# Optimization experiments

Hardware: AMD Instinct MI355X
Metric: run time of the kernel (lower is better)

Reference implementation:

```python
import jax, jax.numpy as jnp
import numpy as np

D_MODEL = 1024
N_HEADS = 16
HEAD_DIM = D_MODEL // N_HEADS


def setup_inputs() -> dict:
    key = jax.random.key(0)
    ks = jax.random.split(key, 9)
    B, T, S, D = 4, 2048, 512, D_MODEL
    sc = 1.0 / np.sqrt(D)
    return {
        "x": jax.random.normal(ks[0], (B, T, D), dtype=jnp.float32),
        "context": jax.random.normal(ks[1], (B, S, D), dtype=jnp.float32),
        "context_mask": jnp.ones((B, S), dtype=bool),
        "Wq": jax.random.normal(ks[2], (D, D), dtype=jnp.float32) * sc,
        "bq": jnp.zeros((D,), dtype=jnp.float32),
        "Wkv": jax.random.normal(ks[3], (D, 2 * D), dtype=jnp.float32) * sc,
        "bkv": jnp.zeros((2 * D,), dtype=jnp.float32),
        "Wp": jax.random.normal(ks[4], (D, D), dtype=jnp.float32) * sc,
        "bp": jnp.zeros((D,), dtype=jnp.float32),
    }


def reference(x, context, context_mask, Wq, bq, Wkv, bkv, Wp, bp):
    B, T, D = x.shape
    S = context.shape[1]
    H, Hd = N_HEADS, HEAD_DIM
    # projections
    q = (x @ Wq + bq).reshape(B, T, H, Hd).transpose(0, 2, 1, 3)          # [B,H,T,Hd]
    kv = (context @ Wkv + bkv).reshape(B, S, 2, H, Hd)
    k = kv[:, :, 0].transpose(0, 2, 1, 3)                                  # [B,H,S,Hd]
    v = kv[:, :, 1].transpose(0, 2, 1, 3)                                  # [B,H,S,Hd]
    # scaled dot-product attention with context mask
    scores = jnp.einsum("bhtd,bhsd->bhts", q, k) / np.sqrt(Hd)            # [B,H,T,S]
    neg_inf = jnp.finfo(scores.dtype).min
    scores = jnp.where(context_mask[:, None, None, :], scores, neg_inf)
    attn = jax.nn.softmax(scores, axis=-1)
    # dropout is identity in eval mode (p applied only in training)
    out = jnp.einsum("bhts,bhsd->bthd", attn, v).reshape(B, T, D)
    return out @ Wp + bp
```

## Files before the change

kernel.cpp:

```cpp
#include <hip/hip_runtime.h>

typedef __bf16 bf16x8 __attribute__((ext_vector_type(8)));
typedef float  f32x4  __attribute__((ext_vector_type(4)));
typedef float  f32x16 __attribute__((ext_vector_type(16)));
typedef unsigned int u32x2 __attribute__((ext_vector_type(2)));

#define MFMA(a, b, c)   __builtin_amdgcn_mfma_f32_16x16x32_bf16((a), (b), (c), 0, 0, 0)
#define MFMA32(a, b, c) __builtin_amdgcn_mfma_f32_32x32x16_bf16((a), (b), (c), 0, 0, 0)

#define GLL(g, l) __builtin_amdgcn_global_load_lds(                                  \
    (const __attribute__((address_space(1))) void*)(g),                              \
    (__attribute__((address_space(3))) void*)(l), 16, 0, 0)

#define BB 4
#define TT 2048
#define SS 512
#define DM 1024
#define NH 16
#define HD 64

__device__ __forceinline__ unsigned short f2bh(float f) {
    __bf16 h = (__bf16)f;
    union { __bf16 h; unsigned short u; } v; v.h = h;
    return v.u;
}

__device__ __forceinline__ unsigned int pk2(float a, float b) {
    return (unsigned int)f2bh(a) | ((unsigned int)f2bh(b) << 16);
}

__device__ __forceinline__ void pl32swap(unsigned int& a, unsigned int& b) {
    u32x2 r = __builtin_amdgcn_permlane32_swap(a, b, false, false);
    a = r[0]; b = r[1];
}

__device__ __forceinline__ float fexp2(float x) {
    float e;
    asm("v_exp_f32 %0, %1" : "=v"(e) : "v"(x));
    return e;
}

__device__ __forceinline__ void tcast_tile(const float* __restrict__ in,
                                           unsigned short* __restrict__ out,
                                           int K, int N, int n0, int k0,
                                           float (*tile)[33], int tid) {
    int tx = tid & 31, ty = tid >> 5;
#pragma unroll
    for (int r = 0; r < 32; r += 8)
        tile[ty + r][tx] = in[(k0 + ty + r) * N + n0 + tx];
    __syncthreads();
    int r2 = tid >> 3, cg = (tid & 7) * 4;
    ushort4 o;
    o.x = f2bh(tile[cg + 0][r2]);
    o.y = f2bh(tile[cg + 1][r2]);
    o.z = f2bh(tile[cg + 2][r2]);
    o.w = f2bh(tile[cg + 3][r2]);
    *(ushort4*)&out[(n0 + r2) * K + k0 + cg] = o;
}

__global__ __launch_bounds__(256)
void prep(const float4* __restrict__ x, const float4* __restrict__ ctx,
          const unsigned int* __restrict__ mw,
          const float* __restrict__ Wq, const float* __restrict__ Wkv,
          const float* __restrict__ Wp,
          ushort4* __restrict__ Xbf, ushort4* __restrict__ Cbf,
          unsigned short* __restrict__ WqT, unsigned short* __restrict__ WkvT,
          unsigned short* __restrict__ WpT, float* __restrict__ mbias) {
    __shared__ float tile[32][33];
    __shared__ int flags[2];
    const int bid = blockIdx.x, tid = threadIdx.x;
    if (bid < 8192) {
        int i = bid * 256 + tid;
        float4 v = x[i];
        ushort4 o; o.x = f2bh(v.x); o.y = f2bh(v.y); o.z = f2bh(v.z); o.w = f2bh(v.w);
        Xbf[i] = o;
    } else if (bid < 10240) {
        int i = (bid - 8192) * 256 + tid;
        float4 v = ctx[i];
        ushort4 o; o.x = f2bh(v.x); o.y = f2bh(v.y); o.z = f2bh(v.z); o.w = f2bh(v.w);
        Cbf[i] = o;
    } else if (bid < 11264) {
        int loc = bid - 10240;
        tcast_tile(Wq, WqT, DM, DM, (loc & 31) * 32, (loc >> 5) * 32, tile, tid);
    } else if (bid < 13312) {
        int loc = bid - 11264;
        tcast_tile(Wkv, WkvT, DM, 2 * DM, (loc & 63) * 32, (loc >> 6) * 32, tile, tid);
    } else if (bid < 14336) {
        int loc = bid - 13312;
        tcast_tile(Wp, WpT, DM, DM, (loc & 31) * 32, (loc >> 5) * 32, tile, tid);
    } else {
        if (tid == 0) { flags[0] = 1; flags[1] = 1; }
        __syncthreads();
        int okI = 1, okF = 1;
        for (int i = tid; i < 512; i += 256) {
            unsigned int w = mw[i];
            if (w > 1u) okI = 0;
            if (w != 0u && w != 0x3f800000u) okF = 0;
        }
        if (!okI) atomicAnd(&flags[0], 0);
        if (!okF) atomicAnd(&flags[1], 0);
        __syncthreads();
        bool wordLayout = (flags[0] != 0) || (flags[1] != 0);
        const unsigned char* mb = (const unsigned char*)mw;
        for (int s = tid; s < BB * SS; s += 256) {
            bool on = wordLayout ? (mw[s] != 0u) : (mb[s] != 0);
            mbias[s] = on ? 0.0f : -1e38f;
        }
    }
}

__device__ __forceinline__ void gemm_core(
    const unsigned short* __restrict__ A, const unsigned short* __restrict__ Bt,
    int K, int m0, int n0, unsigned short* As, unsigned short* Bs,
    f32x4 (*acc)[4]) {
    const int tid = threadIdx.x;
    const int l = tid & 63;
    const int quad = l >> 4, col = l & 15;
    const int w = tid >> 6;
    const int wm = (w & 1) * 64, wn = (w >> 1) * 64;
    const int arow = tid >> 3;
    const int apiece = (tid & 7) ^ (arow & 7);
    const unsigned short* Ab = A + (size_t)(m0 + arow) * K + apiece * 8;
    const unsigned short* Bb = Bt + (size_t)(n0 + arow) * K + apiece * 8;

    for (int k0 = 0; k0 < K; k0 += 64) {
        __syncthreads();
#pragma unroll
        for (int g = 0; g < 4; ++g)
            GLL(Ab + k0 + g * 32 * K, &As[g * 2048 + tid * 8]);
#pragma unroll
        for (int g = 0; g < 4; ++g)
            GLL(Bb + k0 + g * 32 * K, &Bs[g * 2048 + tid * 8]);
        __syncthreads();
#pragma unroll
        for (int k32 = 0; k32 < 2; ++k32) {
            bf16x8 af[4], bfr[4];
#pragma unroll
            for (int i = 0; i < 4; i++) {
                int rr = wm + i * 16 + col;
                af[i] = *(const bf16x8*)&As[rr * 64 + (((k32 * 4 + quad) ^ (rr & 7)) * 8)];
            }
#pragma unroll
            for (int j = 0; j < 4; j++) {
                int rr = wn + j * 16 + col;
                bfr[j] = *(const bf16x8*)&Bs[rr * 64 + (((k32 * 4 + quad) ^ (rr & 7)) * 8)];
            }
#pragma unroll
            for (int i = 0; i < 4; i++)
#pragma unroll
                for (int j = 0; j < 4; j++) acc[i][j] = MFMA(af[i], bfr[j], acc[i][j]);
        }
    }
}

__global__ __launch_bounds__(256, 3)
void gemm_qkv(const unsigned short* __restrict__ Xbf, const unsigned short* __restrict__ WqT,
              const float* __restrict__ bq, unsigned short* __restrict__ Qb,
              const unsigned short* __restrict__ Cbf, const unsigned short* __restrict__ WkvT,
              const float* __restrict__ bkv, unsigned short* __restrict__ Kb,
              unsigned short* __restrict__ Vtb) {
    __shared__ __align__(16) unsigned short S[16640];
    unsigned short* As = S;
    unsigned short* Bs = S + 8192;
    const int tid = threadIdx.x;
    const int l = tid & 63;
    const int quad = l >> 4, col = l & 15;
    const int w = tid >> 6;
    const int wm = (w & 1) * 64, wn = (w >> 1) * 64;
    const int bid = blockIdx.x;

    const f32x4 zero = {0.f, 0.f, 0.f, 0.f};
    f32x4 acc[4][4];
#pragma unroll
    for (int i = 0; i < 4; i++)
#pragma unroll
        for (int j = 0; j < 4; j++) acc[i][j] = zero;

    if (bid < 512) {
        const int xg = bid & 7, t = bid >> 3;
        const int m0 = (xg + 8 * (t & 7)) * 128;
        const int n0 = (t >> 3) * 128;
        gemm_core(Xbf, WqT, DM, m0, n0, As, Bs, acc);
        const float QS = 0.125f * 1.4426950408889634f;
#pragma unroll
        for (int i = 0; i < 4; i++) {
#pragma unroll
            for (int j = 0; j < 4; j++) {
                int n = n0 + wn + j * 16 + col;
                int mb = m0 + wm + i * 16 + quad * 4;
                float bv = bq[n];
#pragma unroll
                for (int ii = 0; ii < 4; ii++)
                    Qb[(mb + ii) * DM + n] = f2bh((acc[i][j][ii] + bv) * QS);
            }
        }
    } else {
        const int loc = bid - 512;
        const int xg = loc & 7, t = loc >> 3;
        const int m0 = (xg + 8 * (t & 1)) * 128;
        const int n0 = (t >> 1) * 128;
        gemm_core(Cbf, WkvT, DM, m0, n0, As, Bs, acc);
        if (n0 < 1024) {
#pragma unroll
            for (int i = 0; i < 4; i++) {
#pragma unroll
                for (int j = 0; j < 4; j++) {
                    int n = n0 + wn + j * 16 + col;
                    int mb = m0 + wm + i * 16 + quad * 4;
                    float bv = bkv[n];
                    int h = n >> 6, d = n & 63;
#pragma unroll
                    for (int ii = 0; ii < 4; ii++) {
                        int m = mb + ii; int b = m >> 9, s = m & 511;
                        Kb[(((b * NH + h) * SS) + s) * HD + d] = f2bh(acc[ii == ii ? i : i][j][ii] + bv);
                    }
                }
            }
        } else {
            __syncthreads();
#pragma unroll
            for (int i = 0; i < 4; i++) {
#pragma unroll
                for (int j = 0; j < 4; j++) {
                    int nl = wn + j * 16 + col;
                    int ml = wm + i * 16 + quad * 4;
                    float bv = bkv[n0 + nl];
#pragma unroll
                    for (int ii = 0; ii < 4; ii++)
                        S[(ml + ii) * 130 + nl] = f2bh(acc[i][j][ii] + bv);
                }
            }
            __syncthreads();
            const int nl = tid >> 1, sc = (tid & 1) * 64;
            const int q = n0 - 1024 + nl;
            const int h = q >> 6, d = q & 63;
            const int b = m0 >> 9;
            unsigned short* vrow = Vtb + (((size_t)(b * NH + h) * HD) + d) * SS
                                       + (m0 & 511) + sc;
#pragma unroll
            for (int k = 0; k < 64; k += 4) {
                ushort4 o;
                o.x = S[(sc + k + 0) * 130 + nl];
                o.y = S[(sc + k + 1) * 130 + nl];
                o.z = S[(sc + k + 2) * 130 + nl];
                o.w = S[(sc + k + 3) * 130 + nl];
                *(ushort4*)&vrow[k] = o;
            }
        }
    }
}

__global__ __launch_bounds__(256, 3)
void gemm_out(const unsigned short* __restrict__ Ob, const unsigned short* __restrict__ WpT,
              const float* __restrict__ bp, float* __restrict__ out) {
    __shared__ __align__(16) unsigned short As[128 * 64];
    __shared__ __align__(16) unsigned short Bs[128 * 64];
    const int tid = threadIdx.x;
    const int l = tid & 63;
    const int quad = l >> 4, col = l & 15;
    const int w = tid >> 6;
    const int wm = (w & 1) * 64, wn = (w >> 1) * 64;
    const int bid = blockIdx.x;
    const int xg = bid & 7, t = bid >> 3;
    const int m0 = (xg + 8 * (t & 7)) * 128;
    const int n0 = (t >> 3) * 128;

    const f32x4 zero = {0.f, 0.f, 0.f, 0.f};
    f32x4 acc[4][4];
#pragma unroll
    for (int i = 0; i < 4; i++)
#pragma unroll
        for (int j = 0; j < 4; j++) acc[i][j] = zero;

    gemm_core(Ob, WpT, DM, m0, n0, As, Bs, acc);

#pragma unroll
    for (int i = 0; i < 4; i++) {
#pragma unroll
        for (int j = 0; j < 4; j++) {
            int n = n0 + wn + j * 16 + col;
            int mb = m0 + wm + i * 16 + quad * 4;
            float bv = bp[n];
#pragma unroll
            for (int ii = 0; ii < 4; ii++)
                out[(mb + ii) * DM + n] = acc[i][j][ii] + bv;
        }
    }
}

__global__ __launch_bounds__(256, 4)
void flash_attn(const unsigned short* __restrict__ Q, const unsigned short* __restrict__ Kb,
                const unsigned short* __restrict__ Vt, const float* __restrict__ mbias,
                unsigned short* __restrict__ O) {
    const int bid = blockIdx.x;
    const int xg = bid & 7, tq = bid >> 3;
    const int tb = tq & 15;
    const int bh = xg + 8 * (tq >> 4);
    const int b = bh >> 4;
    const int tid = threadIdx.x;
    const int w = tid >> 6, l = tid & 63;
    const int lq = l & 31, hi = l >> 5;

    __shared__ __align__(16) unsigned short Ks[2][64 * 64];
    __shared__ __align__(16) unsigned short Vs[2][64 * 64];
    __shared__ float biasS[SS];

    const unsigned short* Kh = Kb + bh * SS * HD;
    const unsigned short* Vh = Vt + bh * HD * SS;

    float bv0 = mbias[b * SS + tid];
    float bv1 = mbias[b * SS + 256 + tid];
    biasS[tid] = bv0; biasS[tid + 256] = bv1;
    const int allon = __syncthreads_and((bv0 == 0.0f) && (bv1 == 0.0f));

    const int rowbase = b * TT + tb * 128 + w * 32;
    const int hd0 = (bh & 15) * HD;

    const unsigned short* qrow = Q + (size_t)(rowbase + lq) * DM + hd0;
    bf16x8 qf[4];
#pragma unroll
    for (int ch = 0; ch < 4; ++ch)
        qf[ch] = *(const bf16x8*)(qrow + ch * 16 + hi * 8);

    const int r0 = tid >> 3, sp = tid & 7;
    const int r1 = r0 + 32;
    const int kgo0 = r0 * HD + ((sp ^ (r0 & 7)) * 8);
    const int kgo1 = r1 * HD + ((sp ^ (r1 & 7)) * 8);
    const int vgo0 = r0 * SS + ((sp ^ (r0 & 7)) * 8);
    const int vgo1 = r1 * SS + ((sp ^ (r1 & 7)) * 8);

    GLL(Kh + kgo0, &Ks[0][tid * 8]);
    GLL(Kh + kgo1, &Ks[0][2048 + tid * 8]);
    GLL(Vh + vgo0, &Vs[0][tid * 8]);
    GLL(Vh + vgo1, &Vs[0][2048 + tid * 8]);

    const f32x16 zero16 = {0.f,0.f,0.f,0.f,0.f,0.f,0.f,0.f,
                           0.f,0.f,0.f,0.f,0.f,0.f,0.f,0.f};
    f32x16 oacc0 = zero16, oacc1 = zero16;
    float lsum = 0.f;

    for (int it = 0; it < SS / 64; ++it) {
        const int s0 = it * 64;
        const int buf = it & 1;
        __syncthreads();
        if (it + 1 < SS / 64) {
            GLL(Kh + (s0 + 64) * HD + kgo0, &Ks[buf ^ 1][tid * 8]);
            GLL(Kh + (s0 + 64) * HD + kgo1, &Ks[buf ^ 1][2048 + tid * 8]);
            GLL(Vh + (s0 + 64) + vgo0, &Vs[buf ^ 1][tid * 8]);
            GLL(Vh + (s0 + 64) + vgo1, &Vs[buf ^ 1][2048 + tid * 8]);
        }

#pragma unroll
        for (int t = 0; t < 2; ++t) {
            const int rk = lq + 32 * t;
            f32x16 cs = zero16;
            __builtin_amdgcn_s_setprio(1);
#pragma unroll
            for (int ch = 0; ch < 4; ++ch) {
                bf16x8 kf = *(const bf16x8*)&Ks[buf][rk * 64 + (((2 * ch + hi) ^ (lq & 7)) * 8)];
                cs = MFMA32(kf, qf[ch], cs);
            }
            __builtin_amdgcn_s_setprio(0);

            float pr[16];
#pragma unroll
            for (int r = 0; r < 16; ++r) {
                float sc = cs[r];
                if (!allon)
                    sc += biasS[s0 + 32 * t + ((r & 3) + 8 * (r >> 2) + 4 * hi)];
                pr[r] = fexp2(sc);
            }
            lsum += ((pr[0] + pr[1]) + (pr[2] + pr[3])) + ((pr[4] + pr[5]) + (pr[6] + pr[7]))
                  + ((pr[8] + pr[9]) + (pr[10] + pr[11])) + ((pr[12] + pr[13]) + (pr[14] + pr[15]));
            unsigned int wd0 = pk2(pr[0], pr[1]),   wd1 = pk2(pr[2], pr[3]);
            unsigned int wd2 = pk2(pr[4], pr[5]),   wd3 = pk2(pr[6], pr[7]);
            unsigned int wd4 = pk2(pr[8], pr[9]),   wd5 = pk2(pr[10], pr[11]);
            unsigned int wd6 = pk2(pr[12], pr[13]), wd7 = pk2(pr[14], pr[15]);
            pl32swap(wd0, wd2); pl32swap(wd1, wd3);
            pl32swap(wd4, wd6); pl32swap(wd5, wd7);
            union { unsigned int u[4]; bf16x8 v; } f0, f1;
            f0.u[0] = wd0; f0.u[1] = wd1; f0.u[2] = wd2; f0.u[3] = wd3;
            f1.u[0] = wd4; f1.u[1] = wd5; f1.u[2] = wd6; f1.u[3] = wd7;
            bf16x8 pfrag[2];
            pfrag[0] = f0.v;
            pfrag[1] = f1.v;

            __builtin_amdgcn_s_setprio(1);
#pragma unroll
            for (int win = 0; win < 2; ++win) {
                const int p = 4 * t + 2 * win + hi;
                bf16x8 v0 = *(const bf16x8*)&Vs[buf][lq * 64 + ((p ^ (lq & 7)) * 8)];
                bf16x8 v1 = *(const bf16x8*)&Vs[buf][(lq + 32) * 64 + ((p ^ (lq & 7)) * 8)];
                oacc0 = MFMA32(pfrag[win], v0, oacc0);
                oacc1 = MFMA32(pfrag[win], v1, oacc1);
            }
            __builtin_amdgcn_s_setprio(0);
        }
    }

    lsum += __shfl_xor(lsum, 32);
    float inv = 1.0f / lsum;
    union { float f; int i; } cv; cv.f = inv;
#pragma unroll
    for (int r = 0; r < 16; ++r) {
        const int qloc = (r & 3) + 8 * (r >> 2) + 4 * hi;
        union { int i; float f; } rv;
        rv.i = __builtin_amdgcn_ds_bpermute(4 * qloc, cv.i);
        const float iq = rv.f;
        unsigned short* orow = O + (size_t)(rowbase + qloc) * DM + hd0 + lq;
        orow[0]  = f2bh(oacc0[r] * iq);
        orow[32] = f2bh(oacc1[r] * iq);
    }
}

extern "C" void kernel_launch(void* const* d_in, const int* in_sizes, int n_in,
                              void* d_out, int out_size, void* d_ws, size_t ws_size,
                              hipStream_t stream) {
    const float* x    = (const float*)d_in[0];
    const float* ctx  = (const float*)d_in[1];
    const void*  cmsk = d_in[2];
    const float* Wq   = (const float*)d_in[3];
    const float* bq   = (const float*)d_in[4];
    const float* Wkv  = (const float*)d_in[5];
    const float* bkv  = (const float*)d_in[6];
    const float* Wp   = (const float*)d_in[7];
    const float* bp   = (const float*)d_in[8];
    float* out = (float*)d_out;

    char* ws = (char*)d_ws;
    size_t off = 0;
    auto alloc = [&](size_t bytes) -> void* {
        void* p = ws + off;
        off += (bytes + 255) & ~(size_t)255;
        return p;
    };
    const size_t NX = (size_t)BB * TT * DM;
    const size_t NC = (size_t)BB * SS * DM;
    unsigned short* Xbf  = (unsigned short*)alloc(NX * 2);
    unsigned short* Cbf  = (unsigned short*)alloc(NC * 2);
    unsigned short* WqT  = (unsigned short*)alloc((size_t)DM * DM * 2);
    unsigned short* WkvT = (unsigned short*)alloc((size_t)DM * 2 * DM * 2);
    unsigned short* WpT  = (unsigned short*)alloc((size_t)DM * DM * 2);
    unsigned short* Qb   = (unsigned short*)alloc(NX * 2);
    unsigned short* Kbf  = (unsigned short*)alloc(NC * 2);
    unsigned short* Vtb  = (unsigned short*)alloc(NC * 2);
    unsigned short* Ob   = (unsigned short*)alloc(NX * 2);
    float* mbias         = (float*)alloc((size_t)BB * SS * 4);

    prep<<<14337, 256, 0, stream>>>((const float4*)x, (const float4*)ctx,
                                    (const unsigned int*)cmsk, Wq, Wkv, Wp,
                                    (ushort4*)Xbf, (ushort4*)Cbf,
                                    WqT, WkvT, WpT, mbias);

    gemm_qkv<<<768, 256, 0, stream>>>(Xbf, WqT, bq, Qb, Cbf, WkvT, bkv, Kbf, Vtb);

    flash_attn<<<BB * NH * (TT / 128), 256, 0, stream>>>(Qb, Kbf, Vtb, mbias, Ob);

    gemm_out<<<512, 256, 0, stream>>>(Ob, WpT, bp, out);
}
```

Before: 190.2 us.

## Fuse Q projection into flash attention and shrink projection GEMM to KV only

The Q projection moves out of the combined QKV GEMM and into the attention kernel. Each attention block now computes its own 128x64 Q tile from bf16 X and the transposed Wq, staging through the K/V shared buffers, then packs the result straight into MFMA operand registers. This removes the Q round-trip through global memory and one large GEMM tile set. The cost is that the attention kernel does a K=1024 reduction with a simple, unpipelined load-sync-compute loop, and Wq is re-read by many blocks.

```diff
diff --git a/kernel.cpp b/kernel.cpp
--- a/kernel.cpp
+++ b/kernel.cpp
@@ -154,11 +154,9 @@
 }
 
 __global__ __launch_bounds__(256, 3)
-void gemm_qkv(const unsigned short* __restrict__ Xbf, const unsigned short* __restrict__ WqT,
-              const float* __restrict__ bq, unsigned short* __restrict__ Qb,
-              const unsigned short* __restrict__ Cbf, const unsigned short* __restrict__ WkvT,
-              const float* __restrict__ bkv, unsigned short* __restrict__ Kb,
-              unsigned short* __restrict__ Vtb) {
+void gemm_kv(const unsigned short* __restrict__ Cbf, const unsigned short* __restrict__ WkvT,
+             const float* __restrict__ bkv, unsigned short* __restrict__ Kb,
+             unsigned short* __restrict__ Vtb) {
     __shared__ __align__(16) unsigned short S[16640];
     unsigned short* As = S;
     unsigned short* Bs = S + 8192;
@@ -167,7 +165,10 @@
     const int quad = l >> 4, col = l & 15;
     const int w = tid >> 6;
     const int wm = (w & 1) * 64, wn = (w >> 1) * 64;
-    const int bid = blockIdx.x;
+    const int loc = blockIdx.x;
+    const int xg = loc & 7, t = loc >> 3;
+    const int m0 = (xg + 8 * (t & 1)) * 128;
+    const int n0 = (t >> 1) * 128;
 
     const f32x4 zero = {0.f, 0.f, 0.f, 0.f};
     f32x4 acc[4][4];
@@ -176,76 +177,53 @@
 #pragma unroll
         for (int j = 0; j < 4; j++) acc[i][j] = zero;
 
-    if (bid < 512) {
-        const int xg = bid & 7, t = bid >> 3;
-        const int m0 = (xg + 8 * (t & 7)) * 128;
-        const int n0 = (t >> 3) * 128;
-        gemm_core(Xbf, WqT, DM, m0, n0, As, Bs, acc);
-        const float QS = 0.125f * 1.4426950408889634f;
+    gemm_core(Cbf, WkvT, DM, m0, n0, As, Bs, acc);
+
+    if (n0 < 1024) {
 #pragma unroll
         for (int i = 0; i < 4; i++) {
 #pragma unroll
             for (int j = 0; j < 4; j++) {
                 int n = n0 + wn + j * 16 + col;
                 int mb = m0 + wm + i * 16 + quad * 4;
-                float bv = bq[n];
+                float bv = bkv[n];
+                int h = n >> 6, d = n & 63;
+#pragma unroll
+                for (int ii = 0; ii < 4; ii++) {
+                    int m = mb + ii; int b = m >> 9, s = m & 511;
+                    Kb[(((b * NH + h) * SS) + s) * HD + d] = f2bh(acc[i][j][ii] + bv);
+                }
+            }
+        }
+    } else {
+        __syncthreads();
+#pragma unroll
+        for (int i = 0; i < 4; i++) {
+#pragma unroll
+            for (int j = 0; j < 4; j++) {
+                int nl = wn + j * 16 + col;
+                int ml = wm + i * 16 + quad * 4;
+                float bv = bkv[n0 + nl];
 #pragma unroll
                 for (int ii = 0; ii < 4; ii++)
-                    Qb[(mb + ii) * DM + n] = f2bh((acc[i][j][ii] + bv) * QS);
-            }
-        }
-    } else {
-        const int loc = bid - 512;
-        const int xg = loc & 7, t = loc >> 3;
-        const int m0 = (xg + 8 * (t & 1)) * 128;
-        const int n0 = (t >> 1) * 128;
-        gemm_core(Cbf, WkvT, DM, m0, n0, As, Bs, acc);
-        if (n0 < 1024) {
-#pragma unroll
-            for (int i = 0; i < 4; i++) {
-#pragma unroll
-                for (int j = 0; j < 4; j++) {
-                    int n = n0 + wn + j * 16 + col;
-                    int mb = m0 + wm + i * 16 + quad * 4;
-                    float bv = bkv[n];
-                    int h = n >> 6, d = n & 63;
-#pragma unroll
-                    for (int ii = 0; ii < 4; ii++) {
-                        int m = mb + ii; int b = m >> 9, s = m & 511;
-                        Kb[(((b * NH + h) * SS) + s) * HD + d] = f2bh(acc[ii == ii ? i : i][j][ii] + bv);
-                    }
-                }
-            }
-        } else {
-            __syncthreads();
-#pragma unroll
-            for (int i = 0; i < 4; i++) {
-#pragma unroll
-                for (int j = 0; j < 4; j++) {
-                    int nl = wn + j * 16 + col;
-                    int ml = wm + i * 16 + quad * 4;
-                    float bv = bkv[n0 + nl];
-#pragma unroll
-                    for (int ii = 0; ii < 4; ii++)
-                        S[(ml + ii) * 130 + nl] = f2bh(acc[i][j][ii] + bv);
-                }
-            }
-            __syncthreads();
-            const int nl = tid >> 1, sc = (tid & 1) * 64;
-            const int q = n0 - 1024 + nl;
-            const int h = q >> 6, d = q & 63;
-            const int b = m0 >> 9;
-            unsigned short* vrow = Vtb + (((size_t)(b * NH + h) * HD) + d) * SS
-                                       + (m0 & 511) + sc;
-#pragma unroll
-            for (int k = 0; k < 64; k += 4) {
-                ushort4 o;
-                o.x = S[(sc + k + 0) * 130 + nl];
-                o.y = S[(sc + k + 1) * 130 + nl];
-                o.z = S[(sc + k + 2) * 130 + nl];
-                o.w = S[(sc + k + 3) * 130 + nl];
-                *(ushort4*)&vrow[k] = o;
-            }
+                    S[(ml + ii) * 130 + nl] = f2bh(acc[i][j][ii] + bv);
+            }
+        }
+        __syncthreads();
+        const int nl = tid >> 1, sc = (tid & 1) * 64;
+        const int q = n0 - 1024 + nl;
+        const int h = q >> 6, d = q & 63;
+        const int b = m0 >> 9;
+        unsigned short* vrow = Vtb + (((size_t)(b * NH + h) * HD) + d) * SS
+                                   + (m0 & 511) + sc;
+#pragma unroll
+        for (int k = 0; k < 64; k += 4) {
+            ushort4 o;
+            o.x = S[(sc + k + 0) * 130 + nl];
+            o.y = S[(sc + k + 1) * 130 + nl];
+            o.z = S[(sc + k + 2) * 130 + nl];
+            o.w = S[(sc + k + 3) * 130 + nl];
+            *(ushort4*)&vrow[k] = o;
         }
     }
 }
@@ -289,9 +267,10 @@
 }
 
 __global__ __launch_bounds__(256, 4)
-void flash_attn(const unsigned short* __restrict__ Q, const unsigned short* __restrict__ Kb,
-                const unsigned short* __restrict__ Vt, const float* __restrict__ mbias,
-                unsigned short* __restrict__ O) {
+void flash_attn(const unsigned short* __restrict__ Xbf, const unsigned short* __restrict__ WqT,
+                const float* __restrict__ bq,
+                const unsigned short* __restrict__ Kb, const unsigned short* __restrict__ Vt,
+                const float* __restrict__ mbias, unsigned short* __restrict__ O) {
     const int bid = blockIdx.x;
     const int xg = bid & 7, tq = bid >> 3;
     const int tb = tq & 15;
@@ -304,23 +283,78 @@
     __shared__ __align__(16) unsigned short Ks[2][64 * 64];
     __shared__ __align__(16) unsigned short Vs[2][64 * 64];
     __shared__ float biasS[SS];
+    __shared__ float bqS[64];
 
     const unsigned short* Kh = Kb + bh * SS * HD;
     const unsigned short* Vh = Vt + bh * HD * SS;
+
+    const int rowbase = b * TT + tb * 128 + w * 32;
+    const int qbase = b * TT + tb * 128;
+    const int hd0 = (bh & 15) * HD;
 
     float bv0 = mbias[b * SS + tid];
     float bv1 = mbias[b * SS + 256 + tid];
     biasS[tid] = bv0; biasS[tid + 256] = bv1;
+    if (tid < 64) bqS[tid] = bq[hd0 + tid];
     const int allon = __syncthreads_and((bv0 == 0.0f) && (bv1 == 0.0f));
 
-    const int rowbase = b * TT + tb * 128 + w * 32;
-    const int hd0 = (bh & 15) * HD;
-
-    const unsigned short* qrow = Q + (size_t)(rowbase + lq) * DM + hd0;
+    unsigned short* Xs = &Ks[0][0];
+    unsigned short* Ws = &Vs[0][0];
+    const int arow = tid >> 3;
+    const int apiece = (tid & 7) ^ (arow & 7);
+    const unsigned short* Xb = Xbf + (size_t)(qbase + arow) * DM + apiece * 8;
+    const unsigned short* Wb = WqT + (size_t)(hd0 + arow) * DM + apiece * 8;
+
+    const f32x16 zero16 = {0.f,0.f,0.f,0.f,0.f,0.f,0.f,0.f,
+                           0.f,0.f,0.f,0.f,0.f,0.f,0.f,0.f};
+    f32x16 qaccA = zero16, qaccB = zero16;
+
+    for (int k0 = 0; k0 < DM; k0 += 64) {
+        __syncthreads();
+#pragma unroll
+        for (int g = 0; g < 4; ++g)
+            GLL(Xb + k0 + g * 32 * DM, &Xs[g * 2048 + tid * 8]);
+#pragma unroll
+        for (int g = 0; g < 2; ++g)
+            GLL(Wb + k0 + g * 32 * DM, &Ws[g * 2048 + tid * 8]);
+        __syncthreads();
+        __builtin_amdgcn_s_setprio(1);
+#pragma unroll
+        for (int ch = 0; ch < 4; ++ch) {
+            const int p = ((2 * ch + hi) ^ (lq & 7)) * 8;
+            bf16x8 af0 = *(const bf16x8*)&Ws[lq * 64 + p];
+            bf16x8 af1 = *(const bf16x8*)&Ws[(lq + 32) * 64 + p];
+            bf16x8 bf  = *(const bf16x8*)&Xs[(w * 32 + lq) * 64 + p];
+            qaccA = MFMA32(af0, bf, qaccA);
+            qaccB = MFMA32(af1, bf, qaccB);
+        }
+        __builtin_amdgcn_s_setprio(0);
+    }
+    __syncthreads();
+
+    const float QS = 0.125f * 1.4426950408889634f;
     bf16x8 qf[4];
 #pragma unroll
-    for (int ch = 0; ch < 4; ++ch)
-        qf[ch] = *(const bf16x8*)(qrow + ch * 16 + hi * 8);
+    for (int tile = 0; tile < 2; ++tile) {
+        float pv[16];
+#pragma unroll
+        for (int r = 0; r < 16; ++r) {
+            const int d = (r & 3) + 8 * (r >> 2) + 4 * hi;
+            float av = (tile == 0) ? qaccA[r] : qaccB[r];
+            pv[r] = (av + bqS[32 * tile + d]) * QS;
+        }
+        unsigned int wd0 = pk2(pv[0], pv[1]),   wd1 = pk2(pv[2], pv[3]);
+        unsigned int wd2 = pk2(pv[4], pv[5]),   wd3 = pk2(pv[6], pv[7]);
+        unsigned int wd4 = pk2(pv[8], pv[9]),   wd5 = pk2(pv[10], pv[11]);
+        unsigned int wd6 = pk2(pv[12], pv[13]), wd7 = pk2(pv[14], pv[15]);
+        pl32swap(wd0, wd2); pl32swap(wd1, wd3);
+        pl32swap(wd4, wd6); pl32swap(wd5, wd7);
+        union { unsigned int u[4]; bf16x8 v; } f0, f1;
+        f0.u[0] = wd0; f0.u[1] = wd1; f0.u[2] = wd2; f0.u[3] = wd3;
+        f1.u[0] = wd4; f1.u[1] = wd5; f1.u[2] = wd6; f1.u[3] = wd7;
+        qf[2 * tile + 0] = f0.v;
+        qf[2 * tile + 1] = f1.v;
+    }
 
     const int r0 = tid >> 3, sp = tid & 7;
     const int r1 = r0 + 32;
@@ -334,8 +368,6 @@
     GLL(Vh + vgo0, &Vs[0][tid * 8]);
     GLL(Vh + vgo1, &Vs[0][2048 + tid * 8]);
 
-    const f32x16 zero16 = {0.f,0.f,0.f,0.f,0.f,0.f,0.f,0.f,
-                           0.f,0.f,0.f,0.f,0.f,0.f,0.f,0.f};
     f32x16 oacc0 = zero16, oacc1 = zero16;
     float lsum = 0.f;
 
@@ -441,7 +473,6 @@
     unsigned short* WqT  = (unsigned short*)alloc((size_t)DM * DM * 2);
     unsigned short* WkvT = (unsigned short*)alloc((size_t)DM * 2 * DM * 2);
     unsigned short* WpT  = (unsigned short*)alloc((size_t)DM * DM * 2);
-    unsigned short* Qb   = (unsigned short*)alloc(NX * 2);
     unsigned short* Kbf  = (unsigned short*)alloc(NC * 2);
     unsigned short* Vtb  = (unsigned short*)alloc(NC * 2);
     unsigned short* Ob   = (unsigned short*)alloc(NX * 2);
@@ -452,9 +483,10 @@
                                     (ushort4*)Xbf, (ushort4*)Cbf,
                                     WqT, WkvT, WpT, mbias);
 
-    gemm_qkv<<<768, 256, 0, stream>>>(Xbf, WqT, bq, Qb, Cbf, WkvT, bkv, Kbf, Vtb);
-
-    flash_attn<<<BB * NH * (TT / 128), 256, 0, stream>>>(Qb, Kbf, Vtb, mbias, Ob);
+    gemm_kv<<<256, 256, 0, stream>>>(Cbf, WkvT, bkv, Kbf, Vtb);
+
+    flash_attn<<<BB * NH * (TT / 128), 256, 0, stream>>>(Xbf, WqT, bq, Kbf, Vtb,
+                                                         mbias, Ob);
 
     gemm_out<<<512, 256, 0, stream>>>(Ob, WpT, bp, out);
 }
```

Measured after the change: 210.9 us. +10.9%, slower.
